# Performance work log

Hardware: AMD Instinct MI355X
Metric: run time of the kernel (lower is better)

The kernel has to match this reference:

```python
import jax, jax.numpy as jnp
import numpy as np

K = 20          # neighbors (args.k)
NEG = 0.2       # LeakyReLU slope
EPS = 1e-8      # torch cosine_similarity eps


def knn_idx(x, k):
    # x: [B,C,N] -> idx [B,N,k] of nearest neighbors (largest -dist^2)
    xx = jnp.sum(x * x, axis=1)                       # [B,N]
    inner = jnp.einsum('bcn,bcm->bnm', x, x)          # [B,N,N]
    pd = 2.0 * inner - xx[:, :, None] - xx[:, None, :]
    return jax.lax.top_k(pd, k)[1]


def gather_neighbors(x, idx):
    # x: [B,C,N], idx: [B,N,K] -> [B,N,K,C]
    xt = jnp.transpose(x, (0, 2, 1))
    return jax.vmap(lambda f, i: f[i])(xt, idx)


def lrelu(x):
    return jnp.where(x >= 0, x, NEG * x)


def conv2d_bn(x, W, s, b):
    # 1x1 conv + inference BN (folded into scale s / bias b) + LeakyReLU; x: [B,C,N,K]
    y = jnp.einsum('oc,bcnk->bonk', W, x)
    return lrelu(y * s[None, :, None, None] + b[None, :, None, None])


def conv1d_bn(x, W, s, b):
    y = jnp.einsum('oc,bcn->bon', W, x)
    return lrelu(y * s[None, :, None] + b[None, :, None])


def manifold_weight(xyz, nor):
    # vectorized form of the original per-point double loop:
    # cosine similarity between nearest neighbor's normal (self) and all K neighbor normals
    idx = knn_idx(xyz, K)
    ng = gather_neighbors(nor, idx)                   # [B,N,K,3]
    c = ng[:, :, :1, :]                               # centroid normal [B,N,1,3]
    num = jnp.sum(c * ng, axis=-1)                    # [B,N,K]
    den = jnp.maximum(jnp.linalg.norm(c, axis=-1) * jnp.linalg.norm(ng, axis=-1), EPS)
    return num / den


def edge_stage(x, weight, w_mp, s_mp, b_mp):
    # get_graph_feature(concat=False) * conv_mp(weight), then concat center feats
    B, C, N = x.shape
    idx = knn_idx(x, K)
    neigh = gather_neighbors(x, idx)                  # [B,N,K,C]
    nf = jnp.transpose(neigh - jnp.transpose(x, (0, 2, 1))[:, :, None, :], (0, 3, 1, 2))  # [B,C,N,K]
    w = jnp.broadcast_to(weight[:, None, :, :], (B, C, N, K))
    nf = nf * conv2d_bn(w, w_mp, s_mp, b_mp)
    xc = jnp.broadcast_to(x[:, :, :, None], (B, C, N, K))
    return jnp.concatenate([nf, xc], axis=1)          # [B,2C,N,K]


def setup_inputs() -> dict:
    key = jax.random.key(0)
    keys = jax.random.split(key, 100)
    ki = iter(range(100))
    def nrm(shape, scale):
        return jax.random.normal(keys[next(ki)], shape, jnp.float32) * scale
    B, N = 8, 2048
    inp = {'xyznxnynz': nrm((B, 6, N), 1.0)}
    def add(name, cout, cin):
        inp['w' + name] = nrm((cout, cin), 1.0 / np.sqrt(cin))
        inp['s' + name] = 1.0 + nrm((cout,), 0.1)   # folded BN scale
        inp['b' + name] = nrm((cout,), 0.1)         # folded BN bias
    add('_mp1', 3, 3); add('_mp2', 64, 64); add('_mp3', 64, 64)
    add('1', 64, 6); add('2', 64, 64); add('3', 64, 128); add('4', 64, 64); add('5', 64, 128)
    add('6', 1024, 192); add('7', 256, 1216); add('8', 256, 256); add('9', 128, 256)
    inp['w10'] = nrm((50, 128), 1.0 / np.sqrt(128))
    return inp


def reference(xyznxnynz, w_mp1, s_mp1, b_mp1, w_mp2, s_mp2, b_mp2, w_mp3, s_mp3, b_mp3,
              w1, s1, b1, w2, s2, b2, w3, s3, b3, w4, s4, b4, w5, s5, b5,
              w6, s6, b6, w7, s7, b7, w8, s8, b8, w9, s9, b9, w10):
    xyz = xyznxnynz[:, :3, :]
    nor = xyznxnynz[:, 3:, :]
    N = xyz.shape[2]
    weight = manifold_weight(xyz, nor)                # [B,N,K]

    h = edge_stage(xyz, weight, w_mp1, s_mp1, b_mp1)  # [B,6,N,K]
    h = conv2d_bn(h, w1, s1, b1)
    h = conv2d_bn(h, w2, s2, b2)
    x1 = jnp.max(h, axis=-1)                          # [B,64,N]

    h = edge_stage(x1, weight, w_mp2, s_mp2, b_mp2)   # [B,128,N,K]
    h = conv2d_bn(h, w3, s3, b3)
    h = conv2d_bn(h, w4, s4, b4)
    x2 = jnp.max(h, axis=-1)

    h = edge_stage(x2, weight, w_mp3, s_mp3, b_mp3)
    h = conv2d_bn(h, w5, s5, b5)
    x3 = jnp.max(h, axis=-1)

    x = jnp.concatenate([x1, x2, x3], axis=1)         # [B,192,N]
    x = conv1d_bn(x, w6, s6, b6)                      # [B,1024,N]
    g = jnp.max(x, axis=-1, keepdims=True)
    g = jnp.broadcast_to(g, (g.shape[0], g.shape[1], N))
    x = jnp.concatenate([g, x1, x2, x3], axis=1)      # [B,1216,N]
    x = conv1d_bn(x, w7, s7, b7)
    x = conv1d_bn(x, w8, s8, b8)                      # dropout = identity (eval mode)
    x = conv1d_bn(x, w9, s9, b9)
    return jnp.einsum('oc,bcn->bon', w10, x)          # [B,50,N]
```

## Files before the change

### kernel.cpp

```cpp
#include <hip/hip_runtime.h>
#include <hip/hip_bf16.h>

#define NPT 2048
#define NB 8
#define KNN 20

__device__ __forceinline__ float bf2f(unsigned short u) {
    return __uint_as_float(((unsigned)u) << 16);
}
__device__ __forceinline__ unsigned short f2bf(float f) {
    unsigned u = __float_as_uint(f);
    unsigned lsb = (u >> 16) & 1u;
    u += 0x7fffu + lsb;
    return (unsigned short)(u >> 16);
}
__device__ __forceinline__ float lrelu(float x) { return x >= 0.f ? x : 0.2f * x; }
__device__ __forceinline__ float ldin(const void* p, size_t i, bool f32) {
    return f32 ? ((const float*)p)[i] : bf2f(((const unsigned short*)p)[i]);
}
__device__ __forceinline__ unsigned long long mkkey64(float d, int m) {
    unsigned u = __float_as_uint(d);
    unsigned p = u ^ (unsigned)(((int)u >> 31) | 0x80000000);
    return ((unsigned long long)p << 11) | (unsigned)(2047 - m);
}
__device__ __forceinline__ unsigned long long shfl_xor_u64(unsigned long long v, int off) {
    unsigned lo = (unsigned)__shfl_xor((int)(unsigned)(v & 0xFFFFFFFFull), off);
    unsigned hi = (unsigned)__shfl_xor((int)(unsigned)(v >> 32), off);
    return ((unsigned long long)hi << 32) | lo;
}

constexpr size_t F_IDX1  = 0;
constexpr size_t F_IDX2  = 327680;
constexpr size_t F_WT    = 655360;
constexpr size_t F_XCATT = 983040;
constexpr size_t F_XCAT  = 4128768;
constexpr size_t F_GPART = 7274496;
constexpr size_t F_G     = 7405568;
constexpr size_t F_V7P   = 7413760;
constexpr size_t F_V7    = 7430144;
constexpr size_t F_WP    = 7432192;
constexpr size_t F_FLAG  = 8074048;
constexpr size_t F_XX    = 8074052;
constexpr size_t F_X7    = 0;
constexpr size_t F_X8    = 2097152;
constexpr size_t F_X9    = 4194304;
constexpr size_t F_TOTAL = 8090436;

constexpr size_t P_AMP1 = 0;
constexpr size_t P_BMP1 = 64;
constexpr size_t P_AMP2 = 128;
constexpr size_t P_BMP2 = 192;
constexpr size_t P_AMP3 = 256;
constexpr size_t P_BMP3 = 320;
constexpr size_t P_W1   = 384;
constexpr size_t P_B1   = 896;
constexpr size_t P_W2   = 960;
constexpr size_t P_B2   = 5056;
constexpr size_t P_W3A  = 5120;
constexpr size_t P_W3B  = 9216;
constexpr size_t P_B3   = 13312;
constexpr size_t P_W4   = 13376;
constexpr size_t P_B4   = 17472;
constexpr size_t P_W5A  = 17536;
constexpr size_t P_W5B  = 21632;
constexpr size_t P_B5   = 25728;
constexpr size_t P_W6   = 25792;
constexpr size_t P_B6   = 222400;
constexpr size_t P_W7A  = 223424;
constexpr size_t P_W7B  = 485568;
constexpr size_t P_B7   = 534720;
constexpr size_t P_W8   = 534976;
constexpr size_t P_B8   = 600512;
constexpr size_t P_W9   = 600768;
constexpr size_t P_B9   = 633536;
constexpr size_t P_W10  = 633664;

struct InPtrs { const void* p[38]; };

__global__ __launch_bounds__(256) void zero_out_kernel(unsigned short* out, int nelem) {
    int i = blockIdx.x * 256 + threadIdx.x;
    if (i < nelem) out[i] = 0;
}

__global__ __launch_bounds__(256) void detect_kernel(const unsigned short* __restrict__ u,
                                                     int* __restrict__ flag) {
    __shared__ int red[256];
    int tid = threadIdx.x;
    int cnt = 0;
    for (int i = tid * 2; i < 98304; i += 512) {
        unsigned e = (u[i] >> 7) & 0xFFu;
        cnt += (e == 0xFFu) ? 1 : 0;
    }
    red[tid] = cnt;
    __syncthreads();
    for (int s = 128; s > 0; s >>= 1) {
        if (tid < s) red[tid] += red[tid + s];
        __syncthreads();
    }
    if (tid == 0) flag[0] = (red[0] > 8) ? 1 : 0;
}

__global__ __launch_bounds__(256) void prep_kernel(InPtrs in, float* __restrict__ wp,
                                                   const int* __restrict__ dflag) {
    bool f32 = dflag[0] != 0;
    int gtid = blockIdx.x * 256 + threadIdx.x;
    int gstr = gridDim.x * 256;
    if (gtid < 192) {
        int which = gtid >> 6, o = gtid & 63;
        const void *w, *s, *bb; int cin, cout; size_t ao, bo;
        if (which == 0)      { w = in.p[1]; s = in.p[2]; bb = in.p[3]; cin = 3;  cout = 3;  ao = P_AMP1; bo = P_BMP1; }
        else if (which == 1) { w = in.p[4]; s = in.p[5]; bb = in.p[6]; cin = 64; cout = 64; ao = P_AMP2; bo = P_BMP2; }
        else                 { w = in.p[7]; s = in.p[8]; bb = in.p[9]; cin = 64; cout = 64; ao = P_AMP3; bo = P_BMP3; }
        if (o < cout) {
            float sum = 0.f;
            for (int c = 0; c < cin; c++) sum += ldin(w, o*cin + c, f32);
            wp[ao + o] = sum * ldin(s, o, f32);
            wp[bo + o] = ldin(bb, o, f32);
        }
    }
    for (int i = gtid; i < 512; i += gstr) {
        int q = i & 3, o = (i >> 2) & 63, cc = i >> 8, c = cc*4 + q;
        wp[P_W1 + i] = (c < 6) ? ldin(in.p[10], o*6 + c, f32) * ldin(in.p[11], o, f32) : 0.f;
    }
    for (int i = gtid; i < 64; i += gstr) wp[P_B1 + i] = ldin(in.p[12], i, f32);
    for (int i = gtid; i < 4096; i += gstr) {
        int q = i & 3, o = (i >> 2) & 63, cc = i >> 8;
        wp[P_W2 + i] = ldin(in.p[13], o*64 + cc*4 + q, f32) * ldin(in.p[14], o, f32);
    }
    for (int i = gtid; i < 64; i += gstr) wp[P_B2 + i] = ldin(in.p[15], i, f32);
    for (int i = gtid; i < 4096; i += gstr) {
        int q = i & 3, o = (i >> 2) & 63, cc = i >> 8;
        float sc = ldin(in.p[17], o, f32);
        wp[P_W3A + i] = ldin(in.p[16], o*128 + cc*4 + q, f32) * sc;
        wp[P_W3B + i] = ldin(in.p[16], o*128 + 64 + cc*4 + q, f32) * sc;
    }
    for (int i = gtid; i < 64; i += gstr) wp[P_B3 + i] = ldin(in.p[18], i, f32);
    for (int i = gtid; i < 4096; i += gstr) {
        int q = i & 3, o = (i >> 2) & 63, cc = i >> 8;
        wp[P_W4 + i] = ldin(in.p[19], o*64 + cc*4 + q, f32) * ldin(in.p[20], o, f32);
    }
    for (int i = gtid; i < 64; i += gstr) wp[P_B4 + i] = ldin(in.p[21], i, f32);
    for (int i = gtid; i < 4096; i += gstr) {
        int q = i & 3, o = (i >> 2) & 63, cc = i >> 8;
        float sc = ldin(in.p[23], o, f32);
        wp[P_W5A + i] = ldin(in.p[22], o*128 + cc*4 + q, f32) * sc;
        wp[P_W5B + i] = ldin(in.p[22], o*128 + 64 + cc*4 + q, f32) * sc;
    }
    for (int i = gtid; i < 64; i += gstr) wp[P_B5 + i] = ldin(in.p[24], i, f32);
    for (int i = gtid; i < 192*1024; i += gstr) {
        int o = i & 1023, c = i >> 10;
        wp[P_W6 + i] = ldin(in.p[25], o*192 + c, f32) * ldin(in.p[26], o, f32);
    }
    for (int i = gtid; i < 1024; i += gstr) wp[P_B6 + i] = ldin(in.p[27], i, f32);
    for (int i = gtid; i < 1024*256; i += gstr) {
        int o = i & 255, c = i >> 8;
        wp[P_W7A + i] = ldin(in.p[28], o*1216 + c, f32) * ldin(in.p[29], o, f32);
    }
    for (int i = gtid; i < 192*256; i += gstr) {
        int o = i & 255, c = i >> 8;
        wp[P_W7B + i] = ldin(in.p[28], o*1216 + 1024 + c, f32) * ldin(in.p[29], o, f32);
    }
    for (int i = gtid; i < 256; i += gstr) wp[P_B7 + i] = ldin(in.p[30], i, f32);
    for (int i = gtid; i < 256*256; i += gstr) {
        int o = i & 255, c = i >> 8;
        wp[P_W8 + i] = ldin(in.p[31], o*256 + c, f32) * ldin(in.p[32], o, f32);
    }
    for (int i = gtid; i < 256; i += gstr) wp[P_B8 + i] = ldin(in.p[33], i, f32);
    for (int i = gtid; i < 256*128; i += gstr) {
        int o = i & 127, c = i >> 7;
        wp[P_W9 + i] = ldin(in.p[34], o*256 + c, f32) * ldin(in.p[35], o, f32);
    }
    for (int i = gtid; i < 128; i += gstr) wp[P_B9 + i] = ldin(in.p[36], i, f32);
    for (int i = gtid; i < 128*64; i += gstr) {
        int o = i & 63, c = i >> 6;
        wp[P_W10 + i] = (o < 50) ? ldin(in.p[37], o*128 + c, f32) : 0.f;
    }
}

__global__ __launch_bounds__(256) void knn_xyz_kernel(const void* __restrict__ xin,
                                                      const int* __restrict__ dflag,
                                                      int* __restrict__ idx_out,
                                                      float* __restrict__ wt_out) {
    bool f32 = dflag[0] != 0;
    int lane = threadIdx.x & 63, wid = threadIdx.x >> 6;
    int p = blockIdx.x * 4 + wid;
    int b = p >> 11, n = p & 2047;
    size_t eb = (size_t)b * 6 * NPT;
    float cx0 = ldin(xin, eb + n, f32), cx1 = ldin(xin, eb + NPT + n, f32), cx2 = ldin(xin, eb + 2*NPT + n, f32);
    float xxn = __builtin_fmaf(cx2, cx2, __builtin_fmaf(cx1, cx1, cx0*cx0));
    unsigned long long key[32];
    #pragma unroll
    for (int j4 = 0; j4 < 8; j4++) {
        int m0 = j4*256 + lane*4;
        float x0q[4], x1q[4], x2q[4];
        if (f32) {
            const float* xf = (const float*)xin + eb;
            float4 a0 = *(const float4*)(xf + m0);
            float4 a1 = *(const float4*)(xf + NPT + m0);
            float4 a2 = *(const float4*)(xf + 2*NPT + m0);
            x0q[0]=a0.x; x0q[1]=a0.y; x0q[2]=a0.z; x0q[3]=a0.w;
            x1q[0]=a1.x; x1q[1]=a1.y; x1q[2]=a1.z; x1q[3]=a1.w;
            x2q[0]=a2.x; x2q[1]=a2.y; x2q[2]=a2.z; x2q[3]=a2.w;
        } else {
            const unsigned short* xu = (const unsigned short*)xin + eb;
            ushort4 a0 = *(const ushort4*)(xu + m0);
            ushort4 a1 = *(const ushort4*)(xu + NPT + m0);
            ushort4 a2 = *(const ushort4*)(xu + 2*NPT + m0);
            x0q[0]=bf2f(a0.x); x0q[1]=bf2f(a0.y); x0q[2]=bf2f(a0.z); x0q[3]=bf2f(a0.w);
            x1q[0]=bf2f(a1.x); x1q[1]=bf2f(a1.y); x1q[2]=bf2f(a1.z); x1q[3]=bf2f(a1.w);
            x2q[0]=bf2f(a2.x); x2q[1]=bf2f(a2.y); x2q[2]=bf2f(a2.z); x2q[3]=bf2f(a2.w);
        }
        #pragma unroll
        for (int q = 0; q < 4; q++) {
            float x0 = x0q[q], x1 = x1q[q], x2 = x2q[q];
            float inner = __builtin_fmaf(x2, cx2, __builtin_fmaf(x1, cx1, x0*cx0));
            float xxm   = __builtin_fmaf(x2, x2,  __builtin_fmaf(x1, x1,  x0*x0));
            float d = __builtin_fmaf(2.f, inner, -xxn) - xxm;
            key[j4*4 + q] = mkkey64(d, m0 + q);
        }
    }
    unsigned long long kprev = ~0ull;
    int mym = 0;
    #pragma unroll 1
    for (int k = 0; k < KNN; k++) {
        unsigned long long best = 0ull;
        #pragma unroll
        for (int s = 0; s < 32; s++) {
            unsigned long long v = (key[s] < kprev) ? key[s] : 0ull;
            best = v > best ? v : best;
        }
        #pragma unroll
        for (int off = 32; off > 0; off >>= 1) {
            unsigned long long o = shfl_xor_u64(best, off);
            best = o > best ? o : best;
        }
        if (lane == k) mym = 2047 - (int)(best & 2047ull);
        kprev = best;
    }
    if (lane < KNN) idx_out[(size_t)p*KNN + lane] = mym;
    int m0n = __shfl(mym, 0);
    if (lane < KNN) {
        size_t nb0 = eb + 3*NPT;
        float c0 = ldin(xin, nb0 + m0n, f32), c1 = ldin(xin, nb0 + NPT + m0n, f32), c2 = ldin(xin, nb0 + 2*NPT + m0n, f32);
        float g0 = ldin(xin, nb0 + mym, f32), g1 = ldin(xin, nb0 + NPT + mym, f32), g2 = ldin(xin, nb0 + 2*NPT + mym, f32);
        float cn = sqrtf(__builtin_fmaf(c2, c2, __builtin_fmaf(c1, c1, c0*c0)));
        float gn = sqrtf(__builtin_fmaf(g2, g2, __builtin_fmaf(g1, g1, g0*g0)));
        float num = __builtin_fmaf(c2, g2, __builtin_fmaf(c1, g1, c0*g0));
        wt_out[(size_t)p*KNN + lane] = num / fmaxf(cn * gn, 1e-8f);
    }
}

__global__ __launch_bounds__(512) void norms_kernel(const float* __restrict__ xcat, int inRow,
                                                    float* __restrict__ xxg) {
    int t = blockIdx.x * 512 + threadIdx.x;
    int b = t >> 11, m = t & 2047;
    const float* xb = xcat + ((size_t)b*192 + inRow) * NPT + m;
    float s = 0.f;
    #pragma unroll
    for (int c = 0; c < 64; c++) { float v = xb[(size_t)c*NPT]; s = __builtin_fmaf(v, v, s); }
    xxg[t] = s;
}

__global__ __launch_bounds__(512) void knn_feat_kernel(const float* __restrict__ xcat,
        const float* __restrict__ xcatT, const float* __restrict__ xxg,
        int inOff, int* __restrict__ idx_out) {
    __shared__ float xmL[64][132];
    int tid = threadIdx.x, lane = tid & 63, wid = tid >> 6;
    int p = blockIdx.x * 8 + wid;
    int b = p >> 11, n = p & 2047;
    const float* xb = xcat + ((size_t)b*192 + inOff) * NPT;
    const float* qg = xcatT + ((size_t)(b*NPT + n))*192 + inOff;
    float q[64];
    #pragma unroll
    for (int c4 = 0; c4 < 16; c4++) {
        float4 v = *(const float4*)(qg + c4*4);
        q[c4*4+0] = __int_as_float(__builtin_amdgcn_readfirstlane(__float_as_int(v.x)));
        q[c4*4+1] = __int_as_float(__builtin_amdgcn_readfirstlane(__float_as_int(v.y)));
        q[c4*4+2] = __int_as_float(__builtin_amdgcn_readfirstlane(__float_as_int(v.z)));
        q[c4*4+3] = __int_as_float(__builtin_amdgcn_readfirstlane(__float_as_int(v.w)));
    }
    float xxn = xxg[b*2048 + n];
    unsigned long long key[32];
    #pragma unroll
    for (int ch = 0; ch < 16; ch++) {
        __syncthreads();
        #pragma unroll
        for (int i = 0; i < 4; i++) {
            int idx4 = tid + i*512;
            int c = idx4 >> 5, m4 = (idx4 & 31) * 4;
            *(float4*)&xmL[c][m4] = *(const float4*)(xb + (size_t)c*NPT + ch*128 + m4);
        }
        __syncthreads();
        float in0 = 0.f, in1 = 0.f;
        #pragma unroll
        for (int c = 0; c < 64; c++) {
            float2 v = *(const float2*)&xmL[c][2*lane];
            in0 = __builtin_fmaf(q[c], v.x, in0);
            in1 = __builtin_fmaf(q[c], v.y, in1);
        }
        float2 xxv = *(const float2*)&xxg[b*2048 + ch*128 + 2*lane];
        float d0 = __builtin_fmaf(2.f, in0, -xxn) - xxv.x;
        float d1 = __builtin_fmaf(2.f, in1, -xxn) - xxv.y;
        int m0 = ch*128 + 2*lane;
        key[ch*2]   = mkkey64(d0, m0);
        key[ch*2+1] = mkkey64(d1, m0 + 1);
    }
    unsigned long long kprev = ~0ull;
    int mym = 0;
    #pragma unroll 1
    for (int k = 0; k < KNN; k++) {
        unsigned long long best = 0ull;
        #pragma unroll
        for (int s = 0; s < 32; s++) {
            unsigned long long v = (key[s] < kprev) ? key[s] : 0ull;
            best = v > best ? v : best;
        }
        #pragma unroll
        for (int off = 32; off > 0; off >>= 1) {
            unsigned long long o = shfl_xor_u64(best, off);
            best = o > best ? o : best;
        }
        if (lane == k) mym = 2047 - (int)(best & 2047ull);
        kprev = best;
    }
    if (lane < KNN) idx_out[(size_t)p*KNN + lane] = mym;
}

__global__ __launch_bounds__(128) void stage1_kernel(const void* __restrict__ xin,
        const int* __restrict__ dflag,
        const int* __restrict__ idxb, const float* __restrict__ wtb,
        const float* __restrict__ wp, float* __restrict__ xcat, float* __restrict__ xcatT) {
    __shared__ float y1L[2][KNN][64];
    bool f32 = dflag[0] != 0;
    int lane = threadIdx.x & 63, wid = threadIdx.x >> 6;
    int p = blockIdx.x * 2 + wid, b = p >> 11, n = p & 2047;
    size_t eb = (size_t)b * 6 * NPT;
    float cx0 = ldin(xin, eb + n, f32), cx1 = ldin(xin, eb + NPT + n, f32), cx2 = ldin(xin, eb + 2*NPT + n, f32);
    float aM0 = wp[P_AMP1+0], aM1 = wp[P_AMP1+1], aM2 = wp[P_AMP1+2];
    float bM0 = wp[P_BMP1+0], bM1 = wp[P_BMP1+1], bM2 = wp[P_BMP1+2];
    float w1r[8];
    #pragma unroll
    for (int cc = 0; cc < 2; cc++) {
        float4 v = *(const float4*)&wp[P_W1 + (size_t)(cc*64 + lane)*4];
        w1r[cc*4+0] = v.x; w1r[cc*4+1] = v.y; w1r[cc*4+2] = v.z; w1r[cc*4+3] = v.w;
    }
    float b1v = wp[P_B1 + lane];
    #pragma unroll
    for (int k = 0; k < KNN; k++) {
        int m = idxb[(size_t)p*KNN + k] & 2047;
        float w = wtb[(size_t)p*KNN + k];
        float n0 = ldin(xin, eb + m, f32), n1 = ldin(xin, eb + NPT + m, f32), n2 = ldin(xin, eb + 2*NPT + m, f32);
        float h0 = (n0 - cx0) * lrelu(fmaf(aM0, w, bM0));
        float h1 = (n1 - cx1) * lrelu(fmaf(aM1, w, bM1));
        float h2 = (n2 - cx2) * lrelu(fmaf(aM2, w, bM2));
        float acc = w1r[0]*h0 + w1r[1]*h1 + w1r[2]*h2 + w1r[3]*cx0 + w1r[4]*cx1 + w1r[5]*cx2;
        y1L[wid][k][lane] = lrelu(acc + b1v);
    }
    __syncthreads();
    float acc2[KNN];
    #pragma unroll
    for (int k = 0; k < KNN; k++) acc2[k] = 0.f;
    #pragma unroll
    for (int cc = 0; cc < 16; cc++) {
        float4 w4 = *(const float4*)&wp[P_W2 + (size_t)(cc*64 + lane)*4];
        #pragma unroll
        for (int k = 0; k < KNN; k++) {
            float4 h4 = *(const float4*)&y1L[wid][k][cc*4];
            float a = acc2[k];
            a = fmaf(w4.x, h4.x, a); a = fmaf(w4.y, h4.y, a);
            a = fmaf(w4.z, h4.z, a); a = fmaf(w4.w, h4.w, a);
            acc2[k] = a;
        }
    }
    float b2v = wp[P_B2 + lane];
    float mx = -1e38f;
    #pragma unroll
    for (int k = 0; k < KNN; k++) mx = fmaxf(mx, lrelu(acc2[k] + b2v));
    xcat[((size_t)b*192 + lane)*NPT + n] = mx;
    xcatT[((size_t)(b*NPT + n))*192 + lane] = mx;
}

__global__ __launch_bounds__(128) void stage23_kernel(
        const float* __restrict__ xcatT, const int* __restrict__ idxb, const float* __restrict__ wtb,
        const float* __restrict__ wp,
        int aOff, int bmpOff, int WaOff, int WbOff, int biasOff,
        int W2Off, int bias2Off, int inOff, int outCh, int second,
        float* __restrict__ xcat, float* __restrict__ xcatTo) {
    __shared__ float hL[2][KNN][64];
    __shared__ float cL[2][64];
    int lane = threadIdx.x & 63, wid = threadIdx.x >> 6;
    int p = blockIdx.x * 2 + wid, b = p >> 11, n = p & 2047;
    const float* xTb = xcatT + (size_t)b * NPT * 192 + inOff;
    float cv = xTb[(size_t)n * 192 + lane];
    cL[wid][lane] = cv;
    float aMP = wp[aOff + lane], bMP = wp[bmpOff + lane];
    #pragma unroll
    for (int k = 0; k < KNN; k++) {
        int m = idxb[(size_t)p*KNN + k] & 2047;
        float w = wtb[(size_t)p*KNN + k];
        float nb = xTb[(size_t)m * 192 + lane];
        hL[wid][k][lane] = (nb - cv) * lrelu(fmaf(aMP, w, bMP));
    }
    __syncthreads();
    float vb = 0.f;
    #pragma unroll
    for (int cc = 0; cc < 16; cc++) {
        float4 w4 = *(const float4*)&wp[WbOff + (size_t)(cc*64 + lane)*4];
        float4 c4 = *(const float4*)&cL[wid][cc*4];
        vb = fmaf(w4.x, c4.x, vb); vb = fmaf(w4.y, c4.y, vb);
        vb = fmaf(w4.z, c4.z, vb); vb = fmaf(w4.w, c4.w, vb);
    }
    float acc[KNN];
    #pragma unroll
    for (int k = 0; k < KNN; k++) acc[k] = 0.f;
    #pragma unroll
    for (int cc = 0; cc < 16; cc++) {
        float4 w4 = *(const float4*)&wp[WaOff + (size_t)(cc*64 + lane)*4];
        #pragma unroll
        for (int k = 0; k < KNN; k++) {
            float4 h4 = *(const float4*)&hL[wid][k][cc*4];
            float a = acc[k];
            a = fmaf(w4.x, h4.x, a); a = fmaf(w4.y, h4.y, a);
            a = fmaf(w4.z, h4.z, a); a = fmaf(w4.w, h4.w, a);
            acc[k] = a;
        }
    }
    float bv = wp[biasOff + lane];
    float mx = -1e38f;
    if (second) {
        __syncthreads();
        #pragma unroll
        for (int k = 0; k < KNN; k++) hL[wid][k][lane] = lrelu(acc[k] + vb + bv);
        __syncthreads();
        float acc2[KNN];
        #pragma unroll
        for (int k = 0; k < KNN; k++) acc2[k] = 0.f;
        #pragma unroll
        for (int cc = 0; cc < 16; cc++) {
            float4 w4 = *(const float4*)&wp[W2Off + (size_t)(cc*64 + lane)*4];
            #pragma unroll
            for (int k = 0; k < KNN; k++) {
                float4 h4 = *(const float4*)&hL[wid][k][cc*4];
                float a = acc2[k];
                a = fmaf(w4.x, h4.x, a); a = fmaf(w4.y, h4.y, a);
                a = fmaf(w4.z, h4.z, a); a = fmaf(w4.w, h4.w, a);
                acc2[k] = a;
            }
        }
        float b2v = wp[bias2Off + lane];
        #pragma unroll
        for (int k = 0; k < KNN; k++) mx = fmaxf(mx, lrelu(acc2[k] + b2v));
    } else {
        #pragma unroll
        for (int k = 0; k < KNN; k++) mx = fmaxf(mx, lrelu(acc[k] + vb + bv));
    }
    xcat[((size_t)b*192 + outCh + lane)*NPT + n] = mx;
    xcatTo[((size_t)(b*NPT + n))*192 + outCh + lane] = mx;
}

template<int OUT, bool INBF, bool VBIAS>
__global__ __launch_bounds__(256) void gemm_kernel(
        const void* __restrict__ Xv, const float* __restrict__ WT,
        const float* __restrict__ bias, const float* __restrict__ vbias,
        unsigned short* __restrict__ Ybf, float* __restrict__ Yf,
        const int* __restrict__ dflag,
        int Cin, int strideW, int CoutY) {
    __shared__ float wL[16][68];
    __shared__ float xL[16][132];
    __shared__ float gred[64][17];
    int tid = threadIdx.x;
    int tx = tid & 15, ty = tid >> 4;
    int nt = blockIdx.x * 128, ot = blockIdx.y * 64, b = blockIdx.z;
    const float* Xf = (const float*)Xv;
    const unsigned short* Xs = (const unsigned short*)Xv;
    float acc[4][8];
    #pragma unroll
    for (int i = 0; i < 4; i++)
        #pragma unroll
        for (int j = 0; j < 8; j++) acc[i][j] = 0.f;
    for (int c0 = 0; c0 < Cin; c0 += 16) {
        __syncthreads();
        #pragma unroll
        for (int i = 0; i < 4; i++) {
            int idx = tid + i*256; int r = idx >> 6, o = idx & 63;
            wL[r][o] = WT[(size_t)(c0 + r) * strideW + ot + o];
        }
        #pragma unroll
        for (int i = 0; i < 8; i++) {
            int idx = tid + i*256; int r = idx >> 7, m = idx & 127;
            if (INBF) xL[r][m] = bf2f(Xs[(size_t)b * Cin * NPT + (size_t)(c0 + r) * NPT + nt + m]);
            else      xL[r][m] = Xf[(size_t)b * Cin * NPT + (size_t)(c0 + r) * NPT + nt + m];
        }
        __syncthreads();
        #pragma unroll
        for (int kk = 0; kk < 16; kk++) {
            float4 w4 = *(const float4*)&wL[kk][ty*4];
            float4 xa = *(const float4*)&xL[kk][tx*8];
            float4 xb4 = *(const float4*)&xL[kk][tx*8 + 4];
            float wv[4] = {w4.x, w4.y, w4.z, w4.w};
            float xv[8] = {xa.x, xa.y, xa.z, xa.w, xb4.x, xb4.y, xb4.z, xb4.w};
            #pragma unroll
            for (int oi = 0; oi < 4; oi++)
                #pragma unroll
                for (int j = 0; j < 8; j++)
                    acc[oi][j] = fmaf(wv[oi], xv[j], acc[oi][j]);
        }
    }
    if (OUT == 1) {
        #pragma unroll
        for (int oi = 0; oi < 4; oi++) {
            float bb = bias[ot + ty*4 + oi];
            float m = -1e38f;
            #pragma unroll
            for (int j = 0; j < 8; j++) m = fmaxf(m, lrelu(acc[oi][j] + bb));
            gred[ty*4 + oi][tx] = m;
        }
        __syncthreads();
        if (tid < 64) {
            float m = gred[tid][0];
            #pragma unroll
            for (int t = 1; t < 16; t++) m = fmaxf(m, gred[tid][t]);
            Yf[((size_t)b*16 + blockIdx.x)*1024 + ot + tid] = m;
        }
    } else if (OUT == 2) {
        bool f32 = dflag[0] != 0;
        #pragma unroll
        for (int oi = 0; oi < 4; oi++) {
            int o = ot + ty*4 + oi;
            if (o < 50) {
                size_t base = ((size_t)b*50 + o)*NPT + nt + tx*8;
                #pragma unroll
                for (int j = 0; j < 8; j++) {
                    if (f32) Yf[base + j] = acc[oi][j];
                    else     Ybf[base + j] = f2bf(acc[oi][j]);
                }
            }
        }
    } else {
        #pragma unroll
        for (int oi = 0; oi < 4; oi++) {
            int o = ot + ty*4 + oi;
            float bb = bias[o];
            if (VBIAS) bb += vbias[(size_t)b*256 + o];
            size_t base = ((size_t)b*CoutY + o)*NPT + nt + tx*8;
            #pragma unroll
            for (int j = 0; j < 8; j++) Ybf[base + j] = f2bf(lrelu(acc[oi][j] + bb));
        }
    }
}

__global__ __launch_bounds__(256) void gmax_reduce_kernel(const float* __restrict__ gpart, float* __restrict__ g) {
    int o = blockIdx.x * 256 + threadIdx.x;
    int b = blockIdx.y;
    float m = -1e38f;
    for (int ch = 0; ch < 16; ch++) m = fmaxf(m, gpart[((size_t)b*16 + ch)*1024 + o]);
    g[(size_t)b*1024 + o] = m;
}

__global__ __launch_bounds__(256) void v7_part_kernel(const float* __restrict__ wp, const float* __restrict__ g,
                                                      float* __restrict__ v7p) {
    int o = threadIdx.x, ch = blockIdx.x, b = blockIdx.y;
    __shared__ float gL[128];
    if (threadIdx.x < 128) gL[threadIdx.x] = g[(size_t)b*1024 + ch*128 + threadIdx.x];
    __syncthreads();
    float acc = 0.f;
    #pragma unroll 4
    for (int c = 0; c < 128; c++) acc = fmaf(wp[P_W7A + (size_t)(ch*128 + c)*256 + o], gL[c], acc);
    v7p[((size_t)b*8 + ch)*256 + o] = acc;
}

__global__ __launch_bounds__(256) void v7_sum_kernel(const float* __restrict__ v7p, float* __restrict__ v7) {
    int o = threadIdx.x, b = blockIdx.x;
    float acc = 0.f;
    #pragma unroll
    for (int ch = 0; ch < 8; ch++) acc += v7p[((size_t)b*8 + ch)*256 + o];
    v7[(size_t)b*256 + o] = acc;
}

extern "C" void kernel_launch(void* const* d_in, const int* in_sizes, int n_in,
                              void* d_out, int out_size, void* d_ws, size_t ws_size,
                              hipStream_t stream) {
    (void)in_sizes;
    if (n_in < 38 || ws_size < F_TOTAL * sizeof(float)) {
        int nb = (out_size + 255) / 256;
        hipLaunchKernelGGL(zero_out_kernel, dim3(nb), dim3(256), 0, stream,
                           (unsigned short*)d_out, out_size);
        return;
    }
    float* W = (float*)d_ws;
    InPtrs ptrs;
    for (int i = 0; i < 38; i++) ptrs.p[i] = d_in[i];
    int* idx1 = (int*)(W + F_IDX1);
    int* idx2 = (int*)(W + F_IDX2);
    float* wt = W + F_WT;
    float* xcat = W + F_XCAT;
    float* xcatT = W + F_XCATT;
    unsigned short* x7 = (unsigned short*)(W + F_X7);
    unsigned short* x8 = (unsigned short*)(W + F_X8);
    unsigned short* x9 = (unsigned short*)(W + F_X9);
    float* gpart = W + F_GPART;
    float* g = W + F_G;
    float* v7p = W + F_V7P;
    float* v7 = W + F_V7;
    float* wp = W + F_WP;
    int* dflag = (int*)(W + F_FLAG);
    float* xxg = W + F_XX;

    hipLaunchKernelGGL(detect_kernel, dim3(1), dim3(256), 0, stream,
                       (const unsigned short*)d_in[0], dflag);
    hipLaunchKernelGGL(prep_kernel, dim3(256), dim3(256), 0, stream, ptrs, wp, dflag);
    hipLaunchKernelGGL(knn_xyz_kernel, dim3(4096), dim3(256), 0, stream, d_in[0], dflag, idx1, wt);
    hipLaunchKernelGGL(stage1_kernel, dim3(8192), dim3(128), 0, stream, d_in[0], dflag, idx1, wt, wp, xcat, xcatT);
    hipLaunchKernelGGL(norms_kernel, dim3(32), dim3(512), 0, stream, xcat, 0, xxg);
    hipLaunchKernelGGL(knn_feat_kernel, dim3(2048), dim3(512), 0, stream, xcat, xcatT, xxg, 0, idx2);
    hipLaunchKernelGGL(stage23_kernel, dim3(8192), dim3(128), 0, stream, xcatT, idx2, wt, wp,
        (int)P_AMP2, (int)P_BMP2, (int)P_W3A, (int)P_W3B, (int)P_B3, (int)P_W4, (int)P_B4,
        0, 64, 1, xcat, xcatT);
    hipLaunchKernelGGL(norms_kernel, dim3(32), dim3(512), 0, stream, xcat, 64, xxg);
    hipLaunchKernelGGL(knn_feat_kernel, dim3(2048), dim3(512), 0, stream, xcat, xcatT, xxg, 64, idx2);
    hipLaunchKernelGGL(stage23_kernel, dim3(8192), dim3(128), 0, stream, xcatT, idx2, wt, wp,
        (int)P_AMP3, (int)P_BMP3, (int)P_W5A, (int)P_W5B, (int)P_B5, 0, 0,
        64, 128, 0, xcat, xcatT);
    hipLaunchKernelGGL((gemm_kernel<1,false,false>), dim3(16,16,8), dim3(256), 0, stream,
        (const void*)xcat, wp + P_W6, wp + P_B6, (const float*)nullptr,
        (unsigned short*)nullptr, gpart, dflag, 192, 1024, 1024);
    hipLaunchKernelGGL(gmax_reduce_kernel, dim3(4,8), dim3(256), 0, stream, gpart, g);
    hipLaunchKernelGGL(v7_part_kernel, dim3(8,8), dim3(256), 0, stream, wp, g, v7p);
    hipLaunchKernelGGL(v7_sum_kernel, dim3(8), dim3(256), 0, stream, v7p, v7);
    hipLaunchKernelGGL((gemm_kernel<0,false,true>), dim3(16,4,8), dim3(256), 0, stream,
        (const void*)xcat, wp + P_W7B, wp + P_B7, v7, x7, (float*)nullptr, dflag, 192, 256, 256);
    hipLaunchKernelGGL((gemm_kernel<0,true,false>), dim3(16,4,8), dim3(256), 0, stream,
        (const void*)x7, wp + P_W8, wp + P_B8, (const float*)nullptr, x8, (float*)nullptr, dflag, 256, 256, 256);
    hipLaunchKernelGGL((gemm_kernel<0,true,false>), dim3(16,2,8), dim3(256), 0, stream,
        (const void*)x8, wp + P_W9, wp + P_B9, (const float*)nullptr, x9, (float*)nullptr, dflag, 256, 128, 128);
    hipLaunchKernelGGL((gemm_kernel<2,true,false>), dim3(16,1,8), dim3(256), 0, stream,
        (const void*)x9, wp + P_W10, (const float*)nullptr, (const float*)nullptr,
        (unsigned short*)d_out, (float*)d_out, dflag, 128, 64, 50);
}
```

Before: 1.722 ms.

## Use per-lane top-2 cache in kNN selection, batch index loads, widen blocks

```diff
diff --git a/kernel.cpp b/kernel.cpp
--- a/kernel.cpp
+++ b/kernel.cpp
@@ -27,6 +27,49 @@
     unsigned lo = (unsigned)__shfl_xor((int)(unsigned)(v & 0xFFFFFFFFull), off);
     unsigned hi = (unsigned)__shfl_xor((int)(unsigned)(v >> 32), off);
     return ((unsigned long long)hi << 32) | lo;
+}
+
+__device__ __forceinline__ void select_topk(const unsigned long long* key, int lane, int* mymp) {
+    unsigned long long b1 = 0ull, b2 = 0ull;
+    #pragma unroll
+    for (int s = 0; s < 32; s++) {
+        unsigned long long v = key[s];
+        bool gt1 = v > b1;
+        unsigned long long nb2 = gt1 ? b1 : (v > b2 ? v : b2);
+        b1 = gt1 ? v : b1;
+        b2 = nb2;
+    }
+    unsigned long long lastpop = ~0ull;
+    int mym = 0;
+    #pragma unroll 1
+    for (int k = 0; k < KNN; k++) {
+        unsigned long long best = b1;
+        #pragma unroll
+        for (int off = 32; off > 0; off >>= 1) {
+            unsigned long long o = shfl_xor_u64(best, off);
+            best = o > best ? o : best;
+        }
+        if (lane == k) mym = 2047 - (int)(best & 2047ull);
+        bool won = (b1 == best) && (best != 0ull);
+        if (won) { lastpop = b1; b1 = b2; b2 = 0ull; }
+        bool dirty = won && (b1 == 0ull);
+        if (__ballot(dirty)) {
+            if (dirty) {
+                unsigned long long n1 = 0ull, n2 = 0ull;
+                #pragma unroll
+                for (int s = 0; s < 32; s++) {
+                    unsigned long long v = key[s];
+                    v = (v < lastpop) ? v : 0ull;
+                    bool gt1 = v > n1;
+                    unsigned long long t2 = gt1 ? n1 : (v > n2 ? v : n2);
+                    n1 = gt1 ? v : n1;
+                    n2 = t2;
+                }
+                b1 = n1; b2 = n2;
+            }
+        }
+    }
+    *mymp = mym;
 }
 
 constexpr size_t F_IDX1  = 0;
@@ -219,24 +262,8 @@
             key[j4*4 + q] = mkkey64(d, m0 + q);
         }
     }
-    unsigned long long kprev = ~0ull;
-    int mym = 0;
-    #pragma unroll 1
-    for (int k = 0; k < KNN; k++) {
-        unsigned long long best = 0ull;
-        #pragma unroll
-        for (int s = 0; s < 32; s++) {
-            unsigned long long v = (key[s] < kprev) ? key[s] : 0ull;
-            best = v > best ? v : best;
-        }
-        #pragma unroll
-        for (int off = 32; off > 0; off >>= 1) {
-            unsigned long long o = shfl_xor_u64(best, off);
-            best = o > best ? o : best;
-        }
-        if (lane == k) mym = 2047 - (int)(best & 2047ull);
-        kprev = best;
-    }
+    int mym;
+    select_topk(key, lane, &mym);
     if (lane < KNN) idx_out[(size_t)p*KNN + lane] = mym;
     int m0n = __shfl(mym, 0);
     if (lane < KNN) {
@@ -305,36 +332,25 @@
         key[ch*2]   = mkkey64(d0, m0);
         key[ch*2+1] = mkkey64(d1, m0 + 1);
     }
-    unsigned long long kprev = ~0ull;
-    int mym = 0;
-    #pragma unroll 1
-    for (int k = 0; k < KNN; k++) {
-        unsigned long long best = 0ull;
-        #pragma unroll
-        for (int s = 0; s < 32; s++) {
-            unsigned long long v = (key[s] < kprev) ? key[s] : 0ull;
-            best = v > best ? v : best;
-        }
-        #pragma unroll
-        for (int off = 32; off > 0; off >>= 1) {
-            unsigned long long o = shfl_xor_u64(best, off);
-            best = o > best ? o : best;
-        }
-        if (lane == k) mym = 2047 - (int)(best & 2047ull);
-        kprev = best;
-    }
+    int mym;
+    select_topk(key, lane, &mym);
     if (lane < KNN) idx_out[(size_t)p*KNN + lane] = mym;
 }
 
-__global__ __launch_bounds__(128) void stage1_kernel(const void* __restrict__ xin,
+__global__ __launch_bounds__(256) void stage1_kernel(const void* __restrict__ xin,
         const int* __restrict__ dflag,
         const int* __restrict__ idxb, const float* __restrict__ wtb,
         const float* __restrict__ wp, float* __restrict__ xcat, float* __restrict__ xcatT) {
-    __shared__ float y1L[2][KNN][64];
+    __shared__ float y1L[4][KNN][64];
     bool f32 = dflag[0] != 0;
     int lane = threadIdx.x & 63, wid = threadIdx.x >> 6;
-    int p = blockIdx.x * 2 + wid, b = p >> 11, n = p & 2047;
+    int p = blockIdx.x * 4 + wid, b = p >> 11, n = p & 2047;
     size_t eb = (size_t)b * 6 * NPT;
+    int myidx = 0; float mywt = 0.f;
+    if (lane < KNN) {
+        myidx = idxb[(size_t)p*KNN + lane] & 2047;
+        mywt  = wtb[(size_t)p*KNN + lane];
+    }
     float cx0 = ldin(xin, eb + n, f32), cx1 = ldin(xin, eb + NPT + n, f32), cx2 = ldin(xin, eb + 2*NPT + n, f32);
     float aM0 = wp[P_AMP1+0], aM1 = wp[P_AMP1+1], aM2 = wp[P_AMP1+2];
     float bM0 = wp[P_BMP1+0], bM1 = wp[P_BMP1+1], bM2 = wp[P_BMP1+2];
@@ -347,8 +363,8 @@
     float b1v = wp[P_B1 + lane];
     #pragma unroll
     for (int k = 0; k < KNN; k++) {
-        int m = idxb[(size_t)p*KNN + k] & 2047;
-        float w = wtb[(size_t)p*KNN + k];
+        int m = __shfl(myidx, k);
+        float w = __shfl(mywt, k);
         float n0 = ldin(xin, eb + m, f32), n1 = ldin(xin, eb + NPT + m, f32), n2 = ldin(xin, eb + 2*NPT + m, f32);
         float h0 = (n0 - cx0) * lrelu(fmaf(aM0, w, bM0));
         float h1 = (n1 - cx1) * lrelu(fmaf(aM1, w, bM1));
@@ -380,24 +396,29 @@
     xcatT[((size_t)(b*NPT + n))*192 + lane] = mx;
 }
 
-__global__ __launch_bounds__(128) void stage23_kernel(
+__global__ __launch_bounds__(256) void stage23_kernel(
         const float* __restrict__ xcatT, const int* __restrict__ idxb, const float* __restrict__ wtb,
         const float* __restrict__ wp,
         int aOff, int bmpOff, int WaOff, int WbOff, int biasOff,
         int W2Off, int bias2Off, int inOff, int outCh, int second,
         float* __restrict__ xcat, float* __restrict__ xcatTo) {
-    __shared__ float hL[2][KNN][64];
-    __shared__ float cL[2][64];
+    __shared__ float hL[4][KNN][64];
+    __shared__ float cL[4][64];
     int lane = threadIdx.x & 63, wid = threadIdx.x >> 6;
-    int p = blockIdx.x * 2 + wid, b = p >> 11, n = p & 2047;
+    int p = blockIdx.x * 4 + wid, b = p >> 11, n = p & 2047;
     const float* xTb = xcatT + (size_t)b * NPT * 192 + inOff;
+    int myidx = 0; float mywt = 0.f;
+    if (lane < KNN) {
+        myidx = idxb[(size_t)p*KNN + lane] & 2047;
+        mywt  = wtb[(size_t)p*KNN + lane];
+    }
     float cv = xTb[(size_t)n * 192 + lane];
     cL[wid][lane] = cv;
     float aMP = wp[aOff + lane], bMP = wp[bmpOff + lane];
     #pragma unroll
     for (int k = 0; k < KNN; k++) {
-        int m = idxb[(size_t)p*KNN + k] & 2047;
-        float w = wtb[(size_t)p*KNN + k];
+        int m = __shfl(myidx, k);
+        float w = __shfl(mywt, k);
         float nb = xTb[(size_t)m * 192 + lane];
         hL[wid][k][lane] = (nb - cv) * lrelu(fmaf(aMP, w, bMP));
     }
@@ -610,15 +631,15 @@
                        (const unsigned short*)d_in[0], dflag);
     hipLaunchKernelGGL(prep_kernel, dim3(256), dim3(256), 0, stream, ptrs, wp, dflag);
     hipLaunchKernelGGL(knn_xyz_kernel, dim3(4096), dim3(256), 0, stream, d_in[0], dflag, idx1, wt);
-    hipLaunchKernelGGL(stage1_kernel, dim3(8192), dim3(128), 0, stream, d_in[0], dflag, idx1, wt, wp, xcat, xcatT);
+    hipLaunchKernelGGL(stage1_kernel, dim3(4096), dim3(256), 0, stream, d_in[0], dflag, idx1, wt, wp, xcat, xcatT);
     hipLaunchKernelGGL(norms_kernel, dim3(32), dim3(512), 0, stream, xcat, 0, xxg);
     hipLaunchKernelGGL(knn_feat_kernel, dim3(2048), dim3(512), 0, stream, xcat, xcatT, xxg, 0, idx2);
-    hipLaunchKernelGGL(stage23_kernel, dim3(8192), dim3(128), 0, stream, xcatT, idx2, wt, wp,
+    hipLaunchKernelGGL(stage23_kernel, dim3(4096), dim3(256), 0, stream, xcatT, idx2, wt, wp,
         (int)P_AMP2, (int)P_BMP2, (int)P_W3A, (int)P_W3B, (int)P_B3, (int)P_W4, (int)P_B4,
         0, 64, 1, xcat, xcatT);
     hipLaunchKernelGGL(norms_kernel, dim3(32), dim3(512), 0, stream, xcat, 64, xxg);
     hipLaunchKernelGGL(knn_feat_kernel, dim3(2048), dim3(512), 0, stream, xcat, xcatT, xxg, 64, idx2);
-    hipLaunchKernelGGL(stage23_kernel, dim3(8192), dim3(128), 0, stream, xcatT, idx2, wt, wp,
+    hipLaunchKernelGGL(stage23_kernel, dim3(4096), dim3(256), 0, stream, xcatT, idx2, wt, wp,
         (int)P_AMP3, (int)P_BMP3, (int)P_W5A, (int)P_W5B, (int)P_B5, 0, 0,
         64, 128, 0, xcat, xcatT);
     hipLaunchKernelGGL((gemm_kernel<1,false,false>), dim3(16,16,8), dim3(256), 0, stream,
```

Result: no change. 1.717 ms (-0.3%).
